# Kernel tuning notes

Hardware: AMD Instinct MI355X
Metric: run time of the kernel (lower is better)

The kernel has to match this reference:

```python
import jax, jax.numpy as jnp
import numpy as np

N_NODES = 100000
N_EDGES = 1600000
IN_DIM = 64
OUT_DIM = 64
BN_EPS = 1e-5


def batchnorm(h, gamma, beta):
    # BatchNorm1d in training mode: per-feature batch stats, biased variance
    mean = jnp.mean(h, axis=0)
    var = jnp.mean((h - mean) ** 2, axis=0)
    return gamma * (h - mean) * jax.lax.rsqrt(var + BN_EPS) + beta


def setup_inputs() -> dict:
    key = jax.random.key(0)
    ks = jax.random.split(key, 4)
    x = jax.random.normal(ks[0], (N_NODES, IN_DIM), dtype=jnp.float32)
    edge_index = jax.random.randint(ks[1], (2, N_EDGES), 0, N_NODES, dtype=jnp.int32)
    epsilon = jnp.asarray(0.1, dtype=jnp.float32)
    # Linear weights stored [in, out] (transpose of torch layout)
    W1 = jax.random.normal(ks[2], (IN_DIM, 2 * OUT_DIM), dtype=jnp.float32) * (1.0 / np.sqrt(IN_DIM))
    b1 = jnp.zeros((2 * OUT_DIM,), dtype=jnp.float32)
    g1 = jnp.ones((2 * OUT_DIM,), dtype=jnp.float32)
    be1 = jnp.zeros((2 * OUT_DIM,), dtype=jnp.float32)
    W2 = jax.random.normal(ks[3], (2 * OUT_DIM, OUT_DIM), dtype=jnp.float32) * (1.0 / np.sqrt(2 * OUT_DIM))
    b2 = jnp.zeros((OUT_DIM,), dtype=jnp.float32)
    g2 = jnp.ones((OUT_DIM,), dtype=jnp.float32)
    be2 = jnp.zeros((OUT_DIM,), dtype=jnp.float32)
    return {"x": x, "edge_index": edge_index, "epsilon": epsilon,
            "W1": W1, "b1": b1, "g1": g1, "be1": be1,
            "W2": W2, "b2": b2, "g2": g2, "be2": be2}


def reference(x, edge_index, epsilon, W1, b1, g1, be1, W2, b2, g2, be2):
    src, dst = edge_index[0], edge_index[1]
    # gather messages from src, scatter-add into dst  [N, D]
    neighbor_sum = jnp.zeros_like(x).at[dst].add(x[src])
    combined = (1.0 + epsilon) * x + neighbor_sum
    h = combined @ W1 + b1            # [N, 2*out_dim]
    h = jax.nn.relu(batchnorm(h, g1, be1))
    h = h @ W2 + b2                   # [N, out_dim]
    return batchnorm(h, g2, be2)
```

## Files before the change

### kernel.cpp

```cpp
#include <hip/hip_runtime.h>

#define N_NODES 100000
#define N_EDGES 1600000
#define IN_DIM 64
#define H_DIM 128
#define OUT_DIM 64
#define BN_EPS 1e-5f
#define CAP 64
#define BIN_SHIFT 7
#define BIN_NODES 128
#define NBINS 782
#define BINCAP 3072
#define OFF_XB     0
#define OFF_BINNED 9600000
#define OFF_COMB   15000000
#define OFF_H1     18200000
#define OFF_H2     24600000
#define OFF_STATS  28000000
#define S1SUM 0
#define S1SQ  128
#define S2SUM 256
#define S2SQ  320

#define DEV_ATOMIC_ADD(p, v) __hip_atomic_fetch_add((p), (v), __ATOMIC_RELAXED, __HIP_MEMORY_SCOPE_AGENT)

typedef __attribute__((ext_vector_type(8))) short short8;
typedef __attribute__((ext_vector_type(4))) float f32x4;

__device__ __forceinline__ unsigned short f2bf(float f) {
  union { float f; unsigned u; } v; v.f = f;
  unsigned r = v.u + 0x7FFFu + ((v.u >> 16) & 1u);
  return (unsigned short)(r >> 16);
}
__device__ __forceinline__ float bflo(unsigned v) { union { unsigned u; float f; } t; t.u = v << 16; return t.f; }
__device__ __forceinline__ float bfhi(unsigned v) { union { unsigned u; float f; } t; t.u = v & 0xFFFF0000u; return t.f; }

__device__ __forceinline__ void acc8(float* a, uint4 v) {
  a[0] += bflo(v.x); a[1] += bfhi(v.x); a[2] += bflo(v.y); a[3] += bfhi(v.y);
  a[4] += bflo(v.z); a[5] += bfhi(v.z); a[6] += bflo(v.w); a[7] += bfhi(v.w);
}
__device__ __forceinline__ uint4 pack8(const float* a) {
  uint4 o;
  o.x = (unsigned)f2bf(a[0]) | ((unsigned)f2bf(a[1]) << 16);
  o.y = (unsigned)f2bf(a[2]) | ((unsigned)f2bf(a[3]) << 16);
  o.z = (unsigned)f2bf(a[4]) | ((unsigned)f2bf(a[5]) << 16);
  o.w = (unsigned)f2bf(a[6]) | ((unsigned)f2bf(a[7]) << 16);
  return o;
}

__global__ __launch_bounds__(256) void k_bsplit(const float* __restrict__ x,
                                                unsigned short* __restrict__ xb,
                                                const int* __restrict__ ei,
                                                int* __restrict__ bcnt,
                                                int* __restrict__ binned) {
  __shared__ int lcnt[NBINS];
  __shared__ int lbase[NBINS];
  const int tid = threadIdx.x;
  for (int i = tid; i < NBINS; i += 256) lcnt[i] = 0;
  #pragma unroll
  for (int j = 0; j < 8; ++j) {
    int i = blockIdx.x * 2048 + j * 256 + tid;
    if (i < N_NODES * IN_DIM / 4) {
      float4 v = ((const float4*)x)[i];
      ushort4 o;
      o.x = f2bf(v.x); o.y = f2bf(v.y); o.z = f2bf(v.z); o.w = f2bf(v.w);
      *(ushort4*)(xb + i * 4) = o;
    }
  }
  __syncthreads();
  int src[8], dst[8], rk[8];
  #pragma unroll
  for (int j = 0; j < 8; ++j) {
    int e = blockIdx.x * 2048 + j * 256 + tid;
    if (e < N_EDGES) {
      src[j] = ei[e];
      dst[j] = ei[N_EDGES + e];
      rk[j] = atomicAdd(&lcnt[dst[j] >> BIN_SHIFT], 1);
    } else {
      src[j] = -1;
    }
  }
  __syncthreads();
  for (int i = tid; i < NBINS; i += 256)
    if (lcnt[i] > 0) lbase[i] = DEV_ATOMIC_ADD(&bcnt[i], lcnt[i]);
  __syncthreads();
  #pragma unroll
  for (int j = 0; j < 8; ++j) {
    if (src[j] >= 0) {
      int b = dst[j] >> BIN_SHIFT;
      int pos = lbase[b] + rk[j];
      if (pos < BINCAP)
        binned[b * BINCAP + pos] = (src[j] << BIN_SHIFT) | (dst[j] & (BIN_NODES - 1));
    }
  }
}

__global__ __launch_bounds__(512) void k_bingather(const unsigned short* __restrict__ xb,
                                                   const float* __restrict__ eps,
                                                   const int* __restrict__ bcnt,
                                                   const int* __restrict__ binned,
                                                   unsigned short* __restrict__ comb) {
  __shared__ int lcnt[BIN_NODES];
  __shared__ int slds[BIN_NODES * CAP];
  const int tid = threadIdx.x;
  const int b = blockIdx.x;
  for (int i = tid; i < BIN_NODES; i += 512) lcnt[i] = 0;
  __syncthreads();
  int n = bcnt[b];
  if (n > BINCAP) n = BINCAP;
  const int* run = binned + b * BINCAP;
  for (int i = tid; i < n; i += 512) {
    int p = run[i];
    int lid = p & (BIN_NODES - 1);
    int pos = atomicAdd(&lcnt[lid], 1);
    if (pos < CAP) slds[lid * CAP + pos] = p >> BIN_SHIFT;
  }
  __syncthreads();
  const int g = (tid >> 3) & 1;
  const int sub = tid & 7;
  const unsigned short* xs = xb + sub * 8;
  const float e1 = 1.0f + eps[0];
  for (int grp = 0; grp < 4; ++grp) {
    int nl = grp * 32 + (tid >> 4);
    int node = b * BIN_NODES + nl;
    if (node >= N_NODES) continue;

    float a[8];
    #pragma unroll
    for (int i = 0; i < 8; ++i) a[i] = 0.f;
    if (g == 0) {
      uint4 sv = *(const uint4*)(xb + (size_t)node * 64 + sub * 8);
      a[0] = bflo(sv.x) * e1; a[1] = bfhi(sv.x) * e1;
      a[2] = bflo(sv.y) * e1; a[3] = bfhi(sv.y) * e1;
      a[4] = bflo(sv.z) * e1; a[5] = bfhi(sv.z) * e1;
      a[6] = bflo(sv.w) * e1; a[7] = bfhi(sv.w) * e1;
    }
    int deg = lcnt[nl];
    if (deg > CAP) deg = CAP;
    const int* sl = slds + nl * CAP;

    int j = g * 4;
    while (j + 12 <= deg) {
      uint4 i0 = *(const uint4*)(sl + j);
      uint4 i1 = *(const uint4*)(sl + j + 8);
      uint4 r0 = *(const uint4*)(xs + (size_t)i0.x * 64);
      uint4 r1 = *(const uint4*)(xs + (size_t)i0.y * 64);
      uint4 r2 = *(const uint4*)(xs + (size_t)i0.z * 64);
      uint4 r3 = *(const uint4*)(xs + (size_t)i0.w * 64);
      uint4 r4 = *(const uint4*)(xs + (size_t)i1.x * 64);
      uint4 r5 = *(const uint4*)(xs + (size_t)i1.y * 64);
      uint4 r6 = *(const uint4*)(xs + (size_t)i1.z * 64);
      uint4 r7 = *(const uint4*)(xs + (size_t)i1.w * 64);
      acc8(a, r0); acc8(a, r1); acc8(a, r2); acc8(a, r3);
      acc8(a, r4); acc8(a, r5); acc8(a, r6); acc8(a, r7);
      j += 16;
    }
    if (j + 4 <= deg) {
      uint4 i0 = *(const uint4*)(sl + j);
      uint4 r0 = *(const uint4*)(xs + (size_t)i0.x * 64);
      uint4 r1 = *(const uint4*)(xs + (size_t)i0.y * 64);
      uint4 r2 = *(const uint4*)(xs + (size_t)i0.z * 64);
      uint4 r3 = *(const uint4*)(xs + (size_t)i0.w * 64);
      acc8(a, r0); acc8(a, r1); acc8(a, r2); acc8(a, r3);
    }
    if (g == ((deg >> 2) & 1)) {
      for (int k = deg & ~3; k < deg; ++k) {
        int s0 = sl[k];
        uint4 r = *(const uint4*)(xs + (size_t)s0 * 64);
        acc8(a, r);
      }
    }
    #pragma unroll
    for (int i = 0; i < 8; ++i) a[i] += __shfl_xor(a[i], 8);
    if (g == 0) *(uint4*)(comb + (size_t)node * 64 + sub * 8) = pack8(a);
  }
}

#define APAD 72
__global__ __launch_bounds__(256) void k_gemm1(const unsigned short* __restrict__ comb,
                                               const float* __restrict__ W1,
                                               const float* __restrict__ b1,
                                               unsigned short* __restrict__ h1,
                                               float* __restrict__ stats) {
  __shared__ unsigned short As[128 * APAD];
  __shared__ unsigned short Ws[128 * APAD];
  __shared__ float red[4][128];
  const int tid = threadIdx.x;
  const int wv = tid >> 6, lane = tid & 63;
  const int quad = lane >> 4, ln = lane & 15;
  const int rowBase = blockIdx.x * 128;

  #pragma unroll
  for (int it = 0; it < 8; ++it) {
    int idx = it * 256 + tid;
    int k = idx >> 5, n4 = idx & 31;
    float4 wv1 = *(const float4*)(W1 + k * 128 + n4 * 4);
    Ws[(n4 * 4 + 0) * APAD + k] = f2bf(wv1.x);
    Ws[(n4 * 4 + 1) * APAD + k] = f2bf(wv1.y);
    Ws[(n4 * 4 + 2) * APAD + k] = f2bf(wv1.z);
    Ws[(n4 * 4 + 3) * APAD + k] = f2bf(wv1.w);
  }
  #pragma unroll
  for (int it = 0; it < 4; ++it) {
    int idx = it * 256 + tid;
    int row = idx >> 3, ch = idx & 7;
    int g = rowBase * 8 + idx;
    uint4 u = (g < N_NODES * 8) ? ((const uint4*)comb)[g] : make_uint4(0, 0, 0, 0);
    *(uint4*)&As[row * APAD + ch * 8] = u;
  }
  __syncthreads();

  f32x4 acc[2][8];
  #pragma unroll
  for (int mt = 0; mt < 2; ++mt) {
    #pragma unroll
    for (int nt = 0; nt < 8; ++nt) acc[mt][nt] = (f32x4)0.0f;
  }
  const int rw = wv * 32;
  #pragma unroll
  for (int kb = 0; kb < 2; ++kb) {
    short8 a0 = *(short8*)&As[(rw + ln) * APAD + kb * 32 + quad * 8];
    short8 a1 = *(short8*)&As[(rw + 16 + ln) * APAD + kb * 32 + quad * 8];
    #pragma unroll
    for (int nt = 0; nt < 8; ++nt) {
      short8 b = *(short8*)&Ws[(nt * 16 + ln) * APAD + kb * 32 + quad * 8];
      acc[0][nt] = __builtin_amdgcn_mfma_f32_16x16x32_bf16(a0, b, acc[0][nt], 0, 0, 0);
      acc[1][nt] = __builtin_amdgcn_mfma_f32_16x16x32_bf16(a1, b, acc[1][nt], 0, 0, 0);
    }
  }

  float bias[8], s[8], q[8];
  #pragma unroll
  for (int nt = 0; nt < 8; ++nt) { bias[nt] = b1[nt * 16 + ln]; s[nt] = 0.f; q[nt] = 0.f; }
  #pragma unroll
  for (int mt = 0; mt < 2; ++mt) {
    #pragma unroll
    for (int i = 0; i < 4; ++i) {
      int gRow = rowBase + rw + mt * 16 + quad * 4 + i;
      if (gRow < N_NODES) {
        #pragma unroll
        for (int nt = 0; nt < 8; ++nt) {
          float v = acc[mt][nt][i] + bias[nt];
          h1[gRow * 128 + nt * 16 + ln] = f2bf(v);
          s[nt] += v; q[nt] += v * v;
        }
      }
    }
  }
  #pragma unroll
  for (int nt = 0; nt < 8; ++nt) {
    s[nt] += __shfl_xor(s[nt], 16); s[nt] += __shfl_xor(s[nt], 32);
    q[nt] += __shfl_xor(q[nt], 16); q[nt] += __shfl_xor(q[nt], 32);
  }
  if (lane < 16) {
    #pragma unroll
    for (int nt = 0; nt < 8; ++nt) red[wv][nt * 16 + ln] = s[nt];
  }
  __syncthreads();
  if (tid < 128) DEV_ATOMIC_ADD(&stats[S1SUM + tid],
                                red[0][tid] + red[1][tid] + red[2][tid] + red[3][tid]);
  __syncthreads();
  if (lane < 16) {
    #pragma unroll
    for (int nt = 0; nt < 8; ++nt) red[wv][nt * 16 + ln] = q[nt];
  }
  __syncthreads();
  if (tid < 128) DEV_ATOMIC_ADD(&stats[S1SQ + tid],
                                red[0][tid] + red[1][tid] + red[2][tid] + red[3][tid]);
}

#define WPAD 136
__global__ __launch_bounds__(256) void k_gemm2(const unsigned short* __restrict__ h1,
                                               const float* __restrict__ W2,
                                               const float* __restrict__ b2,
                                               const float* __restrict__ g1,
                                               const float* __restrict__ be1,
                                               unsigned short* __restrict__ h2,
                                               float* __restrict__ stats) {
  __shared__ unsigned short As[128 * APAD];
  __shared__ unsigned short Ws[64 * WPAD];
  __shared__ float red[4][64];
  __shared__ float scL[128], shL[128];
  const int tid = threadIdx.x;
  const int wv = tid >> 6, lane = tid & 63;
  const int quad = lane >> 4, ln = lane & 15;
  const int rowBase = blockIdx.x * 128;

  if (tid < 128) {
    float mean = stats[S1SUM + tid] * (1.0f / N_NODES);
    float var = stats[S1SQ + tid] * (1.0f / N_NODES) - mean * mean;
    var = fmaxf(var, 0.0f);
    float sc = g1[tid] * rsqrtf(var + BN_EPS);
    scL[tid] = sc;
    shL[tid] = be1[tid] - mean * sc;
  }
  #pragma unroll
  for (int it = 0; it < 8; ++it) {
    int idx = it * 256 + tid;
    int k = idx >> 4, n4 = idx & 15;
    float4 wv2 = *(const float4*)(W2 + k * 64 + n4 * 4);
    Ws[(n4 * 4 + 0) * WPAD + k] = f2bf(wv2.x);
    Ws[(n4 * 4 + 1) * WPAD + k] = f2bf(wv2.y);
    Ws[(n4 * 4 + 2) * WPAD + k] = f2bf(wv2.z);
    Ws[(n4 * 4 + 3) * WPAD + k] = f2bf(wv2.w);
  }

  f32x4 acc[2][4];
  #pragma unroll
  for (int mt = 0; mt < 2; ++mt) {
    #pragma unroll
    for (int nt = 0; nt < 4; ++nt) acc[mt][nt] = (f32x4)0.0f;
  }
  const int rw = wv * 32;

  for (int kc = 0; kc < 2; ++kc) {
    __syncthreads();
    #pragma unroll
    for (int it = 0; it < 4; ++it) {
      int idx = it * 256 + tid;
      int row = idx >> 3, ch = idx & 7;
      int gRow = rowBase + row;
      uint4 u = (gRow < N_NODES) ? *(const uint4*)(h1 + gRow * 128 + kc * 64 + ch * 8)
                                 : make_uint4(0, 0, 0, 0);
      int kb = kc * 64 + ch * 8;
      float f0 = fmaxf(bflo(u.x) * scL[kb + 0] + shL[kb + 0], 0.f);
      float f1 = fmaxf(bfhi(u.x) * scL[kb + 1] + shL[kb + 1], 0.f);
      float f2 = fmaxf(bflo(u.y) * scL[kb + 2] + shL[kb + 2], 0.f);
      float f3 = fmaxf(bfhi(u.y) * scL[kb + 3] + shL[kb + 3], 0.f);
      float f4 = fmaxf(bflo(u.z) * scL[kb + 4] + shL[kb + 4], 0.f);
      float f5 = fmaxf(bfhi(u.z) * scL[kb + 5] + shL[kb + 5], 0.f);
      float f6 = fmaxf(bflo(u.w) * scL[kb + 6] + shL[kb + 6], 0.f);
      float f7 = fmaxf(bfhi(u.w) * scL[kb + 7] + shL[kb + 7], 0.f);
      uint4 o;
      o.x = (unsigned)f2bf(f0) | ((unsigned)f2bf(f1) << 16);
      o.y = (unsigned)f2bf(f2) | ((unsigned)f2bf(f3) << 16);
      o.z = (unsigned)f2bf(f4) | ((unsigned)f2bf(f5) << 16);
      o.w = (unsigned)f2bf(f6) | ((unsigned)f2bf(f7) << 16);
      *(uint4*)&As[row * APAD + ch * 8] = o;
    }
    __syncthreads();
    #pragma unroll
    for (int kb = 0; kb < 2; ++kb) {
      short8 a0 = *(short8*)&As[(rw + ln) * APAD + kb * 32 + quad * 8];
      short8 a1 = *(short8*)&As[(rw + 16 + ln) * APAD + kb * 32 + quad * 8];
      #pragma unroll
      for (int nt = 0; nt < 4; ++nt) {
        short8 b = *(short8*)&Ws[(nt * 16 + ln) * WPAD + kc * 64 + kb * 32 + quad * 8];
        acc[0][nt] = __builtin_amdgcn_mfma_f32_16x16x32_bf16(a0, b, acc[0][nt], 0, 0, 0);
        acc[1][nt] = __builtin_amdgcn_mfma_f32_16x16x32_bf16(a1, b, acc[1][nt], 0, 0, 0);
      }
    }
  }

  float bias[4], s[4], q[4];
  #pragma unroll
  for (int nt = 0; nt < 4; ++nt) { bias[nt] = b2[nt * 16 + ln]; s[nt] = 0.f; q[nt] = 0.f; }
  #pragma unroll
  for (int mt = 0; mt < 2; ++mt) {
    #pragma unroll
    for (int i = 0; i < 4; ++i) {
      int gRow = rowBase + rw + mt * 16 + quad * 4 + i;
      if (gRow < N_NODES) {
        #pragma unroll
        for (int nt = 0; nt < 4; ++nt) {
          float v = acc[mt][nt][i] + bias[nt];
          h2[gRow * 64 + nt * 16 + ln] = f2bf(v);
          s[nt] += v; q[nt] += v * v;
        }
      }
    }
  }
  #pragma unroll
  for (int nt = 0; nt < 4; ++nt) {
    s[nt] += __shfl_xor(s[nt], 16); s[nt] += __shfl_xor(s[nt], 32);
    q[nt] += __shfl_xor(q[nt], 16); q[nt] += __shfl_xor(q[nt], 32);
  }
  if (lane < 16) {
    #pragma unroll
    for (int nt = 0; nt < 4; ++nt) red[wv][nt * 16 + ln] = s[nt];
  }
  __syncthreads();
  if (tid < 64) DEV_ATOMIC_ADD(&stats[S2SUM + tid],
                               red[0][tid] + red[1][tid] + red[2][tid] + red[3][tid]);
  __syncthreads();
  if (lane < 16) {
    #pragma unroll
    for (int nt = 0; nt < 4; ++nt) red[wv][nt * 16 + ln] = q[nt];
  }
  __syncthreads();
  if (tid < 64) DEV_ATOMIC_ADD(&stats[S2SQ + tid],
                               red[0][tid] + red[1][tid] + red[2][tid] + red[3][tid]);
}

__global__ __launch_bounds__(256) void k_out(const unsigned short* __restrict__ h2,
                                             const float* __restrict__ stats,
                                             const float* __restrict__ g2,
                                             const float* __restrict__ be2,
                                             float* __restrict__ out) {
  __shared__ float scL[64], shL[64];
  const int tid = threadIdx.x;
  if (tid < 64) {
    float mean = stats[S2SUM + tid] * (1.0f / N_NODES);
    float var = stats[S2SQ + tid] * (1.0f / N_NODES) - mean * mean;
    var = fmaxf(var, 0.0f);
    float sc = g2[tid] * rsqrtf(var + BN_EPS);
    scL[tid] = sc;
    shL[tid] = be2[tid] - mean * sc;
  }
  __syncthreads();
  int i = blockIdx.x * 256 + tid;
  if (i < N_NODES * OUT_DIM / 4) {
    int c = i & 15;
    uint2 u = *(const uint2*)(h2 + i * 4);
    float4 v = {bflo(u.x), bfhi(u.x), bflo(u.y), bfhi(u.y)};
    float4 sc = ((const float4*)scL)[c];
    float4 sh = ((const float4*)shL)[c];
    v.x = v.x * sc.x + sh.x;
    v.y = v.y * sc.y + sh.y;
    v.z = v.z * sc.z + sh.z;
    v.w = v.w * sc.w + sh.w;
    ((float4*)out)[i] = v;
  }
}

extern "C" void kernel_launch(void* const* d_in, const int* in_sizes, int n_in,
                              void* d_out, int out_size, void* d_ws, size_t ws_size,
                              hipStream_t stream) {
  const float* x   = (const float*)d_in[0];
  const int*   ei  = (const int*)d_in[1];
  const float* eps = (const float*)d_in[2];
  const float* W1  = (const float*)d_in[3];
  const float* b1  = (const float*)d_in[4];
  const float* g1  = (const float*)d_in[5];
  const float* be1 = (const float*)d_in[6];
  const float* W2  = (const float*)d_in[7];
  const float* b2  = (const float*)d_in[8];
  const float* g2  = (const float*)d_in[9];
  const float* be2 = (const float*)d_in[10];

  float* ws = (float*)d_ws;
  unsigned short* xb     = (unsigned short*)(ws + OFF_XB);
  int*            binned = (int*)(ws + OFF_BINNED);
  unsigned short* comb   = (unsigned short*)(ws + OFF_COMB);
  unsigned short* h1     = (unsigned short*)(ws + OFF_H1);
  unsigned short* h2     = (unsigned short*)(ws + OFF_H2);
  float*          stats  = ws + OFF_STATS;
  int*            bcnt   = (int*)(stats + 768);
  float*          out    = (float*)d_out;

  hipMemsetAsync(stats, 0, (768 + NBINS) * sizeof(float), stream);

  const int edgeGrid = (N_EDGES + 2047) / 2048;
  const int gemmGrid = (N_NODES + 127) / 128;
  k_bsplit<<<edgeGrid, 256, 0, stream>>>(x, xb, ei, bcnt, binned);
  k_bingather<<<NBINS, 512, 0, stream>>>(xb, eps, bcnt, binned, comb);
  k_gemm1<<<gemmGrid, 256, 0, stream>>>(comb, W1, b1, h1, stats);
  k_gemm2<<<gemmGrid, 256, 0, stream>>>(h1, W2, b2, g1, be1, h2, stats);
  k_out<<<(N_NODES * OUT_DIM / 4 + 255) / 256, 256, 0, stream>>>(h2, stats, g2, be2, out);
}
```

Measured before the change: 232.1 us.

## Coarsen edge bins to 512 nodes and split each bin across four gather blocks

The edge-binning pass now sorts edges into 256 coarse bins of 512 destination nodes instead of 782 bins of 128, so each block does one global atomic per bin per thread and writes longer contiguous runs. The gather kernel launches four blocks per coarse bin. Each block scans the whole bin but keeps only the edges whose destination falls in its 128-node quarter, so the LDS adjacency layout stays the same. The cost is that every bin's edge list is read four times, and shared-memory atomic contention in the split kernel rises because there are fewer bins.

```diff
diff --git a/kernel.cpp b/kernel.cpp
--- a/kernel.cpp
+++ b/kernel.cpp
@@ -7,10 +7,12 @@
 #define OUT_DIM 64
 #define BN_EPS 1e-5f
 #define CAP 64
-#define BIN_SHIFT 7
-#define BIN_NODES 128
-#define NBINS 782
-#define BINCAP 3072
+#define BIN_SHIFT 9
+#define BIN_NODES 512
+#define NB 256
+#define BINCAP 10240
+#define QNODES 128
+#define NCB 196
 #define OFF_XB     0
 #define OFF_BINNED 9600000
 #define OFF_COMB   15000000
@@ -53,10 +55,10 @@
                                                 const int* __restrict__ ei,
                                                 int* __restrict__ bcnt,
                                                 int* __restrict__ binned) {
-  __shared__ int lcnt[NBINS];
-  __shared__ int lbase[NBINS];
+  __shared__ int lcnt[NB];
+  __shared__ int lbase[NB];
   const int tid = threadIdx.x;
-  for (int i = tid; i < NBINS; i += 256) lcnt[i] = 0;
+  lcnt[tid] = 0;
   #pragma unroll
   for (int j = 0; j < 8; ++j) {
     int i = blockIdx.x * 2048 + j * 256 + tid;
@@ -81,8 +83,7 @@
     }
   }
   __syncthreads();
-  for (int i = tid; i < NBINS; i += 256)
-    if (lcnt[i] > 0) lbase[i] = DEV_ATOMIC_ADD(&bcnt[i], lcnt[i]);
+  if (lcnt[tid] > 0) lbase[tid] = DEV_ATOMIC_ADD(&bcnt[tid], lcnt[tid]);
   __syncthreads();
   #pragma unroll
   for (int j = 0; j < 8; ++j) {
@@ -100,29 +101,34 @@
                                                    const int* __restrict__ bcnt,
                                                    const int* __restrict__ binned,
                                                    unsigned short* __restrict__ comb) {
-  __shared__ int lcnt[BIN_NODES];
-  __shared__ int slds[BIN_NODES * CAP];
+  __shared__ int lcnt[QNODES];
+  __shared__ int slds[QNODES * CAP];
   const int tid = threadIdx.x;
-  const int b = blockIdx.x;
-  for (int i = tid; i < BIN_NODES; i += 512) lcnt[i] = 0;
-  __syncthreads();
-  int n = bcnt[b];
+  const int cb = blockIdx.x >> 2;
+  const int q  = blockIdx.x & 3;
+  if (tid < QNODES) lcnt[tid] = 0;
+  __syncthreads();
+  int n = bcnt[cb];
   if (n > BINCAP) n = BINCAP;
-  const int* run = binned + b * BINCAP;
+  const int* run = binned + cb * BINCAP;
   for (int i = tid; i < n; i += 512) {
     int p = run[i];
     int lid = p & (BIN_NODES - 1);
-    int pos = atomicAdd(&lcnt[lid], 1);
-    if (pos < CAP) slds[lid * CAP + pos] = p >> BIN_SHIFT;
+    if ((lid >> 7) == q) {
+      int nl = lid & (QNODES - 1);
+      int pos = atomicAdd(&lcnt[nl], 1);
+      if (pos < CAP) slds[nl * CAP + pos] = p >> BIN_SHIFT;
+    }
   }
   __syncthreads();
   const int g = (tid >> 3) & 1;
   const int sub = tid & 7;
   const unsigned short* xs = xb + sub * 8;
   const float e1 = 1.0f + eps[0];
+  const int nodeBase = cb * BIN_NODES + q * QNODES;
   for (int grp = 0; grp < 4; ++grp) {
     int nl = grp * 32 + (tid >> 4);
-    int node = b * BIN_NODES + nl;
+    int node = nodeBase + nl;
     if (node >= N_NODES) continue;
 
     float a[8];
@@ -448,12 +454,12 @@
   int*            bcnt   = (int*)(stats + 768);
   float*          out    = (float*)d_out;
 
-  hipMemsetAsync(stats, 0, (768 + NBINS) * sizeof(float), stream);
+  hipMemsetAsync(stats, 0, 1024 * sizeof(float), stream);
 
   const int edgeGrid = (N_EDGES + 2047) / 2048;
   const int gemmGrid = (N_NODES + 127) / 128;
   k_bsplit<<<edgeGrid, 256, 0, stream>>>(x, xb, ei, bcnt, binned);
-  k_bingather<<<NBINS, 512, 0, stream>>>(xb, eps, bcnt, binned, comb);
+  k_bingather<<<NCB * 4, 512, 0, stream>>>(xb, eps, bcnt, binned, comb);
   k_gemm1<<<gemmGrid, 256, 0, stream>>>(comb, W1, b1, h1, stats);
   k_gemm2<<<gemmGrid, 256, 0, stream>>>(h1, W2, b2, g1, be1, h2, stats);
   k_out<<<(N_NODES * OUT_DIM / 4 + 255) / 256, 256, 0, stream>>>(h2, stats, g2, be2, out);
```

Result: no change. 236.4 us (+1.8%).

## Recompute first GEMM in second kernel instead of materializing h1

Applied to the files above, without the earlier changes.

The first GEMM kernel now only accumulates the BatchNorm statistics and no longer writes the 100000x128 bf16 h1 intermediate. The second kernel reloads comb, recomputes the first matmul, applies BN1 and ReLU into shared memory, and feeds the result straight into the second matmul. W2 fragments are now loaded per lane directly from global memory into registers rather than staged through shared memory. This trades the h1 write and read traffic for a repeated first GEMM, and adds register pressure and scattered W2 loads in the second kernel.

```diff
diff --git a/kernel.cpp b/kernel.cpp
--- a/kernel.cpp
+++ b/kernel.cpp
@@ -14,7 +14,6 @@
 #define OFF_XB     0
 #define OFF_BINNED 9600000
 #define OFF_COMB   15000000
-#define OFF_H1     18200000
 #define OFF_H2     24600000
 #define OFF_STATS  28000000
 #define S1SUM 0
@@ -177,11 +176,10 @@
 }
 
 #define APAD 72
-__global__ __launch_bounds__(256) void k_gemm1(const unsigned short* __restrict__ comb,
-                                               const float* __restrict__ W1,
-                                               const float* __restrict__ b1,
-                                               unsigned short* __restrict__ h1,
-                                               float* __restrict__ stats) {
+__global__ __launch_bounds__(256) void k_gemm1s(const unsigned short* __restrict__ comb,
+                                                const float* __restrict__ W1,
+                                                const float* __restrict__ b1,
+                                                float* __restrict__ stats) {
   __shared__ unsigned short As[128 * APAD];
   __shared__ unsigned short Ws[128 * APAD];
   __shared__ float red[4][128];
@@ -241,7 +239,6 @@
         #pragma unroll
         for (int nt = 0; nt < 8; ++nt) {
           float v = acc[mt][nt][i] + bias[nt];
-          h1[gRow * 128 + nt * 16 + ln] = f2bf(v);
           s[nt] += v; q[nt] += v * v;
         }
       }
@@ -269,18 +266,22 @@
                                 red[0][tid] + red[1][tid] + red[2][tid] + red[3][tid]);
 }
 
-#define WPAD 136
-__global__ __launch_bounds__(256) void k_gemm2(const unsigned short* __restrict__ h1,
+#define HP 136
+__global__ __launch_bounds__(256) void k_gemm2(const unsigned short* __restrict__ comb,
+                                               const float* __restrict__ W1,
+                                               const float* __restrict__ b1,
                                                const float* __restrict__ W2,
                                                const float* __restrict__ b2,
                                                const float* __restrict__ g1,
                                                const float* __restrict__ be1,
                                                unsigned short* __restrict__ h2,
                                                float* __restrict__ stats) {
-  __shared__ unsigned short As[128 * APAD];
-  __shared__ unsigned short Ws[64 * WPAD];
+  __shared__ unsigned short smem[2 * 128 * APAD];
   __shared__ float red[4][64];
   __shared__ float scL[128], shL[128];
+  unsigned short* As = smem;
+  unsigned short* Ws1 = smem + 128 * APAD;
+  unsigned short* H = smem;
   const int tid = threadIdx.x;
   const int wv = tid >> 6, lane = tid & 63;
   const int quad = lane >> 4, ln = lane & 15;
@@ -297,57 +298,89 @@
   #pragma unroll
   for (int it = 0; it < 8; ++it) {
     int idx = it * 256 + tid;
-    int k = idx >> 4, n4 = idx & 15;
-    float4 wv2 = *(const float4*)(W2 + k * 64 + n4 * 4);
-    Ws[(n4 * 4 + 0) * WPAD + k] = f2bf(wv2.x);
-    Ws[(n4 * 4 + 1) * WPAD + k] = f2bf(wv2.y);
-    Ws[(n4 * 4 + 2) * WPAD + k] = f2bf(wv2.z);
-    Ws[(n4 * 4 + 3) * WPAD + k] = f2bf(wv2.w);
-  }
-
-  f32x4 acc[2][4];
-  #pragma unroll
-  for (int mt = 0; mt < 2; ++mt) {
-    #pragma unroll
-    for (int nt = 0; nt < 4; ++nt) acc[mt][nt] = (f32x4)0.0f;
+    int k = idx >> 5, n4 = idx & 31;
+    float4 wv1 = *(const float4*)(W1 + k * 128 + n4 * 4);
+    Ws1[(n4 * 4 + 0) * APAD + k] = f2bf(wv1.x);
+    Ws1[(n4 * 4 + 1) * APAD + k] = f2bf(wv1.y);
+    Ws1[(n4 * 4 + 2) * APAD + k] = f2bf(wv1.z);
+    Ws1[(n4 * 4 + 3) * APAD + k] = f2bf(wv1.w);
+  }
+  #pragma unroll
+  for (int it = 0; it < 4; ++it) {
+    int idx = it * 256 + tid;
+    int row = idx >> 3, ch = idx & 7;
+    int g = rowBase * 8 + idx;
+    uint4 u = (g < N_NODES * 8) ? ((const uint4*)comb)[g] : make_uint4(0, 0, 0, 0);
+    *(uint4*)&As[row * APAD + ch * 8] = u;
+  }
+  __syncthreads();
+
+  f32x4 acc1[2][8];
+  #pragma unroll
+  for (int mt = 0; mt < 2; ++mt) {
+    #pragma unroll
+    for (int nt = 0; nt < 8; ++nt) acc1[mt][nt] = (f32x4)0.0f;
   }
   const int rw = wv * 32;
-
+  #pragma unroll
+  for (int kb = 0; kb < 2; ++kb) {
+    short8 a0 = *(short8*)&As[(rw + ln) * APAD + kb * 32 + quad * 8];
+    short8 a1 = *(short8*)&As[(rw + 16 + ln) * APAD + kb * 32 + quad * 8];
+    #pragma unroll
+    for (int nt = 0; nt < 8; ++nt) {
+      short8 b = *(short8*)&Ws1[(nt * 16 + ln) * APAD + kb * 32 + quad * 8];
+      acc1[0][nt] = __builtin_amdgcn_mfma_f32_16x16x32_bf16(a0, b, acc1[0][nt], 0, 0, 0);
+      acc1[1][nt] = __builtin_amdgcn_mfma_f32_16x16x32_bf16(a1, b, acc1[1][nt], 0, 0, 0);
+    }
+  }
+  __syncthreads();
+
+  #pragma unroll
+  for (int mt = 0; mt < 2; ++mt) {
+    #pragma unroll
+    for (int i = 0; i < 4; ++i) {
+      int lRow = rw + mt * 16 + quad * 4 + i;
+      #pragma unroll
+      for (int nt = 0; nt < 8; ++nt) {
+        int c = nt * 16 + ln;
+        float v = acc1[mt][nt][i] + b1[c];
+        v = fmaxf(v * scL[c] + shL[c], 0.f);
+        H[lRow * HP + c] = f2bf(v);
+      }
+    }
+  }
+  __syncthreads();
+
+  f32x4 acc2[2][4];
+  #pragma unroll
+  for (int mt = 0; mt < 2; ++mt) {
+    #pragma unroll
+    for (int nt = 0; nt < 4; ++nt) acc2[mt][nt] = (f32x4)0.0f;
+  }
+  #pragma unroll
   for (int kc = 0; kc < 2; ++kc) {
-    __syncthreads();
-    #pragma unroll
-    for (int it = 0; it < 4; ++it) {
-      int idx = it * 256 + tid;
-      int row = idx >> 3, ch = idx & 7;
-      int gRow = rowBase + row;
-      uint4 u = (gRow < N_NODES) ? *(const uint4*)(h1 + gRow * 128 + kc * 64 + ch * 8)
-                                 : make_uint4(0, 0, 0, 0);
-      int kb = kc * 64 + ch * 8;
-      float f0 = fmaxf(bflo(u.x) * scL[kb + 0] + shL[kb + 0], 0.f);
-      float f1 = fmaxf(bfhi(u.x) * scL[kb + 1] + shL[kb + 1], 0.f);
-      float f2 = fmaxf(bflo(u.y) * scL[kb + 2] + shL[kb + 2], 0.f);
-      float f3 = fmaxf(bfhi(u.y) * scL[kb + 3] + shL[kb + 3], 0.f);
-      float f4 = fmaxf(bflo(u.z) * scL[kb + 4] + shL[kb + 4], 0.f);
-      float f5 = fmaxf(bfhi(u.z) * scL[kb + 5] + shL[kb + 5], 0.f);
-      float f6 = fmaxf(bflo(u.w) * scL[kb + 6] + shL[kb + 6], 0.f);
-      float f7 = fmaxf(bfhi(u.w) * scL[kb + 7] + shL[kb + 7], 0.f);
-      uint4 o;
-      o.x = (unsigned)f2bf(f0) | ((unsigned)f2bf(f1) << 16);
-      o.y = (unsigned)f2bf(f2) | ((unsigned)f2bf(f3) << 16);
-      o.z = (unsigned)f2bf(f4) | ((unsigned)f2bf(f5) << 16);
-      o.w = (unsigned)f2bf(f6) | ((unsigned)f2bf(f7) << 16);
-      *(uint4*)&As[row * APAD + ch * 8] = o;
-    }
-    __syncthreads();
+    short8 wf[4][2];
+    #pragma unroll
+    for (int nt = 0; nt < 4; ++nt) {
+      #pragma unroll
+      for (int kb = 0; kb < 2; ++kb) {
+        short8 f;
+        #pragma unroll
+        for (int j = 0; j < 8; ++j) {
+          int k = kc * 64 + kb * 32 + quad * 8 + j;
+          f[j] = (short)f2bf(W2[k * 64 + nt * 16 + ln]);
+        }
+        wf[nt][kb] = f;
+      }
+    }
     #pragma unroll
     for (int kb = 0; kb < 2; ++kb) {
-      short8 a0 = *(short8*)&As[(rw + ln) * APAD + kb * 32 + quad * 8];
-      short8 a1 = *(short8*)&As[(rw + 16 + ln) * APAD + kb * 32 + quad * 8];
+      short8 a0 = *(short8*)&H[(rw + ln) * HP + kc * 64 + kb * 32 + quad * 8];
+      short8 a1 = *(short8*)&H[(rw + 16 + ln) * HP + kc * 64 + kb * 32 + quad * 8];
       #pragma unroll
       for (int nt = 0; nt < 4; ++nt) {
-        short8 b = *(short8*)&Ws[(nt * 16 + ln) * WPAD + kc * 64 + kb * 32 + quad * 8];
-        acc[0][nt] = __builtin_amdgcn_mfma_f32_16x16x32_bf16(a0, b, acc[0][nt], 0, 0, 0);
-        acc[1][nt] = __builtin_amdgcn_mfma_f32_16x16x32_bf16(a1, b, acc[1][nt], 0, 0, 0);
+        acc2[0][nt] = __builtin_amdgcn_mfma_f32_16x16x32_bf16(a0, wf[nt][kb], acc2[0][nt], 0, 0, 0);
+        acc2[1][nt] = __builtin_amdgcn_mfma_f32_16x16x32_bf16(a1, wf[nt][kb], acc2[1][nt], 0, 0, 0);
       }
     }
   }
@@ -363,7 +396,7 @@
       if (gRow < N_NODES) {
         #pragma unroll
         for (int nt = 0; nt < 4; ++nt) {
-          float v = acc[mt][nt][i] + bias[nt];
+          float v = acc2[mt][nt][i] + bias[nt];
           h2[gRow * 64 + nt * 16 + ln] = f2bf(v);
           s[nt] += v; q[nt] += v * v;
         }
@@ -442,7 +475,6 @@
   unsigned short* xb     = (unsigned short*)(ws + OFF_XB);
   int*            binned = (int*)(ws + OFF_BINNED);
   unsigned short* comb   = (unsigned short*)(ws + OFF_COMB);
-  unsigned short* h1     = (unsigned short*)(ws + OFF_H1);
   unsigned short* h2     = (unsigned short*)(ws + OFF_H2);
   float*          stats  = ws + OFF_STATS;
   int*            bcnt   = (int*)(stats + 768);
@@ -454,7 +486,7 @@
   const int gemmGrid = (N_NODES + 127) / 128;
   k_bsplit<<<edgeGrid, 256, 0, stream>>>(x, xb, ei, bcnt, binned);
   k_bingather<<<NBINS, 512, 0, stream>>>(xb, eps, bcnt, binned, comb);
-  k_gemm1<<<gemmGrid, 256, 0, stream>>>(comb, W1, b1, h1, stats);
-  k_gemm2<<<gemmGrid, 256, 0, stream>>>(h1, W2, b2, g1, be1, h2, stats);
+  k_gemm1s<<<gemmGrid, 256, 0, stream>>>(comb, W1, b1, stats);
+  k_gemm2<<<gemmGrid, 256, 0, stream>>>(comb, W1, b1, W2, b2, g1, be1, h2, stats);
   k_out<<<(N_NODES * OUT_DIM / 4 + 255) / 256, 256, 0, stream>>>(h2, stats, g2, be2, out);
 }
```

Result: slower. 246.9 us (+6.4%).
